# Performance work log

Hardware: AMD Instinct MI355X
Metric: run time of the kernel (lower is better)

The kernel has to match this reference:

```python
import jax, jax.numpy as jnp
import numpy as np

RADIUS = 0.2
MAX_SAMPLES = 9  # matches Conv2d kernel_size=[1, 9]


def ball_query(pcs, radius, nsample):
    """pcs: [B, 3, N] -> group_idx: [B, N, nsample] int32.
    First index of each group is the center point itself (distance 0)."""
    p = jnp.transpose(pcs, (0, 2, 1))  # [B, N, 3]
    sq = jnp.sum(p * p, axis=-1)  # [B, N]
    # pairwise squared distances [B, N, N]
    d2 = sq[:, :, None] + sq[:, None, :] - 2.0 * jnp.einsum('bnd,bmd->bnm', p, p)
    B, N, _ = d2.shape
    idx = jnp.broadcast_to(jnp.arange(N, dtype=jnp.int32), (B, N, N))
    idx = jnp.where(d2 > radius * radius, N, idx)  # out-of-ball -> sentinel N
    idx = jnp.sort(idx, axis=-1)[:, :, :nsample]  # in-ball indices first (ascending)
    first = idx[:, :, 0:1]  # center index (self, d2=0)
    idx = jnp.where(idx == N, first, idx)  # pad with center
    return idx


def setup_inputs() -> dict:
    key = jax.random.key(0)
    k1, k2, k3 = jax.random.split(key, 3)
    B, C_in, C_out, N = 4, 64, 128, 4096
    x = jax.random.normal(k1, (B, C_in, N), dtype=jnp.float32)
    pcs = jax.random.uniform(k2, (B, 3, N), dtype=jnp.float32)
    # Conv2d(in, out, [1, 9]) weight, xavier_uniform; bias zero-init
    fan_in = C_in * 1 * MAX_SAMPLES
    fan_out = C_out * 1 * MAX_SAMPLES
    limit = float(np.sqrt(6.0 / (fan_in + fan_out)))
    W = jax.random.uniform(k3, (C_out, C_in, MAX_SAMPLES), dtype=jnp.float32,
                           minval=-limit, maxval=limit)
    b = jnp.zeros((C_out,), dtype=jnp.float32)
    return {"x": x, "pcs": pcs, "W": W, "b": b}


def reference(x, pcs, W, b):
    """x: [B, C_in, N], pcs: [B, 3, N], W: [C_out, C_in, 9], b: [C_out].
    Returns y: [B, C_out, N]."""
    idx = ball_query(pcs, RADIUS, MAX_SAMPLES)  # [B, N, S]
    # gather grouped features: [B, C_in, N, S]
    x_grp = jnp.take_along_axis(x[:, :, None, :], idx[:, None, :, :], axis=3)
    # grouped, center-normalized coordinates (as in _group_points)
    pcs_grp = jnp.take_along_axis(pcs[:, :, None, :], idx[:, None, :, :], axis=3)
    pcs_grp = pcs_grp - pcs[:, :, :, None]  # [B, 3, N, S] (computed for fidelity)
    # Conv2d(in, out, [1, 9]) over [B, C_in, N, S] -> [B, C_out, N]
    y = jnp.einsum('bcns,ocs->bon', x_grp, W) + b[None, :, None]
    return y
```

## Files before the change

### kernel.cpp

```cpp
#include <hip/hip_runtime.h>

#define N_PTS 4096
#define B_SZ 4
#define C_IN 64
#define C_OUT 128
#define NS 9
#define KTOT (C_IN * NS)
#define RAD2 0.04f

typedef __attribute__((ext_vector_type(8))) short bf16x8;
typedef __attribute__((ext_vector_type(4))) float f32x4;

__device__ inline ushort f2bf(float f) {
    union { float f; unsigned u; } v; v.f = f;
    unsigned r = (v.u + 0x7FFF + ((v.u >> 16) & 1)) >> 16;
    return (ushort)r;
}

__device__ inline void gl_lds16(const void* g, void* l) {
    __builtin_amdgcn_global_load_lds(
        (const __attribute__((address_space(1))) unsigned int*)g,
        (__attribute__((address_space(3))) unsigned int*)l, 16, 0, 0);
}

#define LOADG(gi, qx, qy, qz) do {                                          \
    int mbase_ = (gi) * 256 + lane;                                         \
    _Pragma("unroll")                                                       \
    for (int j_ = 0; j_ < 4; ++j_) {                                        \
        int m_ = mbase_ + j_ * 64;                                          \
        qx[j_] = pb[m_]; qy[j_] = pb[N_PTS + m_]; qz[j_] = pb[2 * N_PTS + m_]; \
    }                                                                       \
} while (0)

#define PROCG(gi, qx, qy, qz) do {                                          \
    _Pragma("unroll")                                                       \
    for (int j_ = 0; j_ < 4; ++j_) {                                        \
        int m_ = (gi) * 256 + j_ * 64 + lane;                               \
        float sqm_ = __fadd_rn(__fadd_rn(__fmul_rn(qx[j_], qx[j_]),         \
                                         __fmul_rn(qy[j_], qy[j_])),        \
                               __fmul_rn(qz[j_], qz[j_]));                  \
        float dot_ = __fadd_rn(__fadd_rn(__fmul_rn(cx, qx[j_]),             \
                                         __fmul_rn(cy, qy[j_])),            \
                               __fmul_rn(cz, qz[j_]));                      \
        float d2_ = __fsub_rn(__fadd_rn(csq, sqm_), __fmul_rn(2.0f, dot_)); \
        bool hit_ = !(d2_ > RAD2);                                          \
        unsigned long long mask_ = __ballot(hit_);                          \
        if (mask_) {                                                        \
            if (first < 0) first = (gi) * 256 + j_ * 64 + __ffsll(mask_) - 1; \
            unsigned mlo_ = (unsigned)mask_, mhi_ = (unsigned)(mask_ >> 32); \
            int pre_ = __builtin_amdgcn_mbcnt_hi(mhi_,                      \
                           __builtin_amdgcn_mbcnt_lo(mlo_, 0));             \
            if (hit_) {                                                     \
                int slot_ = cnt + pre_;                                     \
                if (slot_ < NS) outb[(size_t)slot_ * N_PTS] = m_;           \
            }                                                               \
            cnt += __popcll(mask_);                                         \
        }                                                                   \
    }                                                                       \
} while (0)

__global__ void __launch_bounds__(256) prep_kernel(
    const float* __restrict__ W, const float* __restrict__ x,
    const float* __restrict__ pcs,
    ushort* __restrict__ Wt, ushort* __restrict__ xT, int* __restrict__ idxT)
{
    __shared__ ushort tile[64][66];
    const int t = threadIdx.x;
    const int blk = blockIdx.x;

    if (blk < 4096) {
        const int lane = t & 63;
        const int pt = t >> 6;
        const int widp = blk * 4 + pt;
        const int b = widp >> 12;
        const int n = widp & (N_PTS - 1);
        const float* pb = pcs + (size_t)b * 3 * N_PTS;
        float cx = pb[n], cy = pb[N_PTS + n], cz = pb[2 * N_PTS + n];
        float csq = __fadd_rn(__fadd_rn(__fmul_rn(cx, cx), __fmul_rn(cy, cy)),
                              __fmul_rn(cz, cz));
        int* outb = idxT + (size_t)b * NS * N_PTS + n;
        int cnt = 0, first = -1;
        float ax[4], ay[4], az[4], bx[4], by[4], bz[4];
        LOADG(0, ax, ay, az);
        #pragma unroll 1
        for (int g = 0; g < 16; g += 2) {
            if (g + 1 < 16) LOADG(g + 1, bx, by, bz);
            PROCG(g, ax, ay, az);
            if (cnt >= NS) break;
            if (g + 2 < 16) LOADG(g + 2, ax, ay, az);
            PROCG(g + 1, bx, by, bz);
            if (cnt >= NS) break;
        }
        if (lane >= cnt && lane < NS) outb[(size_t)lane * N_PTS] = first;
    } else if (blk < 4384) {
        int id = (blk - 4096) * 256 + t;
        int o = id / KTOT;
        int r = id - o * KTOT;
        int s = r >> 6, c = r & 63;
        int dst = o * KTOT + s * 64 + (((c >> 3) ^ (o & 7)) << 3) + (c & 7);
        Wt[dst] = f2bf(W[o * KTOT + c * NS + s]);
    } else {
        int r = blk - 4384;
        int b = r >> 6;
        int n0 = (r & 63) * 64;
        const float* xb = x + (size_t)b * C_IN * N_PTS;
        #pragma unroll
        for (int i = 0; i < 16; ++i) {
            int flat = i * 256 + t;
            int c = flat >> 6, n = flat & 63;
            tile[c][n] = f2bf(xb[(size_t)c * N_PTS + n0 + n]);
        }
        __syncthreads();
        ushort* xTb = xT + ((size_t)b * N_PTS + n0) * C_IN;
        #pragma unroll
        for (int i = 0; i < 16; ++i) {
            int flat = i * 256 + t;
            int n = flat >> 6, c = flat & 63;
            xTb[(size_t)n * C_IN + c] = tile[c][n];
        }
    }
}

__global__ void __launch_bounds__(512) conv_kernel(
    const ushort* __restrict__ xT, const ushort* __restrict__ Wt,
    const int* __restrict__ idxT, const float* __restrict__ bias,
    float* __restrict__ y)
{
    __shared__ __align__(16) ushort Wlds[64 * KTOT];
    __shared__ __align__(16) ushort Xlds[576 * 64];

    const int t = threadIdx.x;
    const int lane = t & 63;
    const int wid = t >> 6;
    const int ntile = blockIdx.x;
    const int b = blockIdx.y;
    const int n64 = ntile * 64;
    const int l15 = lane & 15;
    const int l4 = lane >> 4;

    const ushort* xTb = xT + (size_t)b * N_PTS * C_IN;
    const int* idxTb = idxT + (size_t)b * NS * N_PTS;

    const int rb = wid * 72;
    int g[9];
    #pragma unroll
    for (int j = 0; j < 9; ++j) {
        int r = rb + j * 8 + (lane >> 3);
        g[j] = idxTb[((r >> 6) << 12) + n64 + (r & 63)];
    }

    #pragma unroll
    for (int j = 0; j < 9; ++j) {
        int off = (wid * 9 + j) * 512 + lane * 8;
        gl_lds16(Wt + off, &Wlds[off]);
    }
    {
        const int sx = (((lane & 7) ^ (lane >> 3)) << 3);
        #pragma unroll
        for (int j = 0; j < 9; ++j)
            gl_lds16(xTb + ((size_t)g[j] << 6) + sx,
                     &Xlds[(rb + j * 8) * 64 + lane * 8]);
    }
    __syncthreads();

    const int m0 = (wid & 1) * 32;
    const int n0w = (wid >> 1) * 16;
    const int ra0 = m0 + l15;
    const int rb0 = n0w + l15;
    const int swA = ra0 & 7;
    const int swB = rb0 & 7;
    float* yb = y + (size_t)b * C_OUT * N_PTS + n64;

    #pragma unroll
    for (int half = 0; half < 2; ++half) {
        f32x4 acc[2];
        acc[0] = (f32x4){0.f, 0.f, 0.f, 0.f};
        acc[1] = (f32x4){0.f, 0.f, 0.f, 0.f};

        #pragma unroll
        for (int s = 0; s < NS; ++s) {
            #pragma unroll
            for (int hh = 0; hh < 2; ++hh) {
                int d = hh * 4 + l4;
                bf16x8 a0 = *(const bf16x8*)&Wlds[ra0 * KTOT + s * 64 + ((d ^ swA) << 3)];
                bf16x8 a1 = *(const bf16x8*)&Wlds[(ra0 + 16) * KTOT + s * 64 + ((d ^ swA) << 3)];
                bf16x8 b0 = *(const bf16x8*)&Xlds[(s * 64 + rb0) * 64 + ((d ^ swB) << 3)];
                acc[0] = __builtin_amdgcn_mfma_f32_16x16x32_bf16(a0, b0, acc[0], 0, 0, 0);
                acc[1] = __builtin_amdgcn_mfma_f32_16x16x32_bf16(a1, b0, acc[1], 0, 0, 0);
            }
        }

        #pragma unroll
        for (int fm = 0; fm < 2; ++fm) {
            #pragma unroll
            for (int j = 0; j < 4; ++j) {
                int o = half * 64 + m0 + fm * 16 + l4 * 4 + j;
                yb[(size_t)o * N_PTS + n0w + l15] = acc[fm][j] + bias[o];
            }
        }

        if (half == 0) {
            __syncthreads();
            #pragma unroll
            for (int j = 0; j < 9; ++j) {
                int off = (wid * 9 + j) * 512 + lane * 8;
                gl_lds16(Wt + 36864 + off, &Wlds[off]);
            }
            __syncthreads();
        }
    }
}

extern "C" void kernel_launch(void* const* d_in, const int* in_sizes, int n_in,
                              void* d_out, int out_size, void* d_ws, size_t ws_size,
                              hipStream_t stream) {
    const float* x    = (const float*)d_in[0];
    const float* pcs  = (const float*)d_in[1];
    const float* W    = (const float*)d_in[2];
    const float* bias = (const float*)d_in[3];
    float* y = (float*)d_out;

    int*    idxT = (int*)d_ws;
    ushort* xT   = (ushort*)((char*)d_ws + 851968);
    ushort* Wt   = (ushort*)((char*)d_ws + 2949120);

    prep_kernel<<<4640, 256, 0, stream>>>(W, x, pcs, Wt, xT, idxT);
    conv_kernel<<<dim3(64, B_SZ), 512, 0, stream>>>(xT, Wt, idxT, bias, y);
}
```

Measured before the change: 20.58 us.

## Precompute packed float4 points with squared norms in a separate ball-query kernel

The prep kernel now packs each point as a float4 (x, y, z, |p|^2) into workspace. Ball query moves into its own kernel that reads these packed points with one vector load and no per-candidate norm computation. This cuts scattered scalar loads and per-candidate arithmetic, at the cost of an extra kernel launch and a dependency between the two kernels. The x transpose and W conversion no longer share a launch with the ball query.

```diff
diff --git a/kernel.cpp b/kernel.cpp
--- a/kernel.cpp
+++ b/kernel.cpp
@@ -23,26 +23,65 @@
         (__attribute__((address_space(3))) unsigned int*)l, 16, 0, 0);
 }
 
-#define LOADG(gi, qx, qy, qz) do {                                          \
+__global__ void __launch_bounds__(256) prep_kernel(
+    const float* __restrict__ W, const float* __restrict__ x,
+    const float* __restrict__ pcs,
+    ushort* __restrict__ Wt, ushort* __restrict__ xT, float4* __restrict__ pp)
+{
+    __shared__ ushort tile[64][66];
+    const int t = threadIdx.x;
+    const int blk = blockIdx.x;
+    if (blk < 288) {
+        int id = blk * 256 + t;
+        int o = id / KTOT;
+        int r = id - o * KTOT;
+        int s = r >> 6, c = r & 63;
+        int dst = o * KTOT + s * 64 + (((c >> 3) ^ (o & 7)) << 3) + (c & 7);
+        Wt[dst] = f2bf(W[o * KTOT + c * NS + s]);
+    } else if (blk < 544) {
+        int r = blk - 288;
+        int b = r >> 6;
+        int n0 = (r & 63) * 64;
+        const float* xb = x + (size_t)b * C_IN * N_PTS;
+        #pragma unroll
+        for (int i = 0; i < 16; ++i) {
+            int flat = i * 256 + t;
+            int c = flat >> 6, n = flat & 63;
+            tile[c][n] = f2bf(xb[(size_t)c * N_PTS + n0 + n]);
+        }
+        __syncthreads();
+        ushort* xTb = xT + ((size_t)b * N_PTS + n0) * C_IN;
+        #pragma unroll
+        for (int i = 0; i < 16; ++i) {
+            int flat = i * 256 + t;
+            int n = flat >> 6, c = flat & 63;
+            xTb[(size_t)n * C_IN + c] = tile[c][n];
+        }
+    } else {
+        int id = (blk - 544) * 256 + t;
+        int b = id >> 12, n = id & (N_PTS - 1);
+        const float* pb = pcs + (size_t)b * 3 * N_PTS;
+        float px = pb[n], py = pb[N_PTS + n], pz = pb[2 * N_PTS + n];
+        float sq = __fadd_rn(__fadd_rn(__fmul_rn(px, px), __fmul_rn(py, py)),
+                             __fmul_rn(pz, pz));
+        pp[id] = make_float4(px, py, pz, sq);
+    }
+}
+
+#define LOADG(gi, q) do {                                                   \
     int mbase_ = (gi) * 256 + lane;                                         \
     _Pragma("unroll")                                                       \
-    for (int j_ = 0; j_ < 4; ++j_) {                                        \
-        int m_ = mbase_ + j_ * 64;                                          \
-        qx[j_] = pb[m_]; qy[j_] = pb[N_PTS + m_]; qz[j_] = pb[2 * N_PTS + m_]; \
-    }                                                                       \
+    for (int j_ = 0; j_ < 4; ++j_) q[j_] = pb4[mbase_ + j_ * 64];           \
 } while (0)
 
-#define PROCG(gi, qx, qy, qz) do {                                          \
+#define PROCG(gi, q) do {                                                   \
     _Pragma("unroll")                                                       \
     for (int j_ = 0; j_ < 4; ++j_) {                                        \
         int m_ = (gi) * 256 + j_ * 64 + lane;                               \
-        float sqm_ = __fadd_rn(__fadd_rn(__fmul_rn(qx[j_], qx[j_]),         \
-                                         __fmul_rn(qy[j_], qy[j_])),        \
-                               __fmul_rn(qz[j_], qz[j_]));                  \
-        float dot_ = __fadd_rn(__fadd_rn(__fmul_rn(cx, qx[j_]),             \
-                                         __fmul_rn(cy, qy[j_])),            \
-                               __fmul_rn(cz, qz[j_]));                      \
-        float d2_ = __fsub_rn(__fadd_rn(csq, sqm_), __fmul_rn(2.0f, dot_)); \
+        float dot_ = __fadd_rn(__fadd_rn(__fmul_rn(cx, q[j_].x),            \
+                                         __fmul_rn(cy, q[j_].y)),           \
+                               __fmul_rn(cz, q[j_].z));                     \
+        float d2_ = __fsub_rn(__fadd_rn(csq, q[j_].w), __fmul_rn(2.0f, dot_)); \
         bool hit_ = !(d2_ > RAD2);                                          \
         unsigned long long mask_ = __ballot(hit_);                          \
         if (mask_) {                                                        \
@@ -59,66 +98,29 @@
     }                                                                       \
 } while (0)
 
-__global__ void __launch_bounds__(256) prep_kernel(
-    const float* __restrict__ W, const float* __restrict__ x,
-    const float* __restrict__ pcs,
-    ushort* __restrict__ Wt, ushort* __restrict__ xT, int* __restrict__ idxT)
-{
-    __shared__ ushort tile[64][66];
-    const int t = threadIdx.x;
-    const int blk = blockIdx.x;
-
-    if (blk < 4096) {
-        const int lane = t & 63;
-        const int pt = t >> 6;
-        const int widp = blk * 4 + pt;
-        const int b = widp >> 12;
-        const int n = widp & (N_PTS - 1);
-        const float* pb = pcs + (size_t)b * 3 * N_PTS;
-        float cx = pb[n], cy = pb[N_PTS + n], cz = pb[2 * N_PTS + n];
-        float csq = __fadd_rn(__fadd_rn(__fmul_rn(cx, cx), __fmul_rn(cy, cy)),
-                              __fmul_rn(cz, cz));
-        int* outb = idxT + (size_t)b * NS * N_PTS + n;
-        int cnt = 0, first = -1;
-        float ax[4], ay[4], az[4], bx[4], by[4], bz[4];
-        LOADG(0, ax, ay, az);
-        #pragma unroll 1
-        for (int g = 0; g < 16; g += 2) {
-            if (g + 1 < 16) LOADG(g + 1, bx, by, bz);
-            PROCG(g, ax, ay, az);
-            if (cnt >= NS) break;
-            if (g + 2 < 16) LOADG(g + 2, ax, ay, az);
-            PROCG(g + 1, bx, by, bz);
-            if (cnt >= NS) break;
-        }
-        if (lane >= cnt && lane < NS) outb[(size_t)lane * N_PTS] = first;
-    } else if (blk < 4384) {
-        int id = (blk - 4096) * 256 + t;
-        int o = id / KTOT;
-        int r = id - o * KTOT;
-        int s = r >> 6, c = r & 63;
-        int dst = o * KTOT + s * 64 + (((c >> 3) ^ (o & 7)) << 3) + (c & 7);
-        Wt[dst] = f2bf(W[o * KTOT + c * NS + s]);
-    } else {
-        int r = blk - 4384;
-        int b = r >> 6;
-        int n0 = (r & 63) * 64;
-        const float* xb = x + (size_t)b * C_IN * N_PTS;
-        #pragma unroll
-        for (int i = 0; i < 16; ++i) {
-            int flat = i * 256 + t;
-            int c = flat >> 6, n = flat & 63;
-            tile[c][n] = f2bf(xb[(size_t)c * N_PTS + n0 + n]);
-        }
-        __syncthreads();
-        ushort* xTb = xT + ((size_t)b * N_PTS + n0) * C_IN;
-        #pragma unroll
-        for (int i = 0; i < 16; ++i) {
-            int flat = i * 256 + t;
-            int n = flat >> 6, c = flat & 63;
-            xTb[(size_t)n * C_IN + c] = tile[c][n];
-        }
-    }
+__global__ void __launch_bounds__(256) ballq_kernel(const float4* __restrict__ pp,
+                                                    int* __restrict__ idxT) {
+    const int lane = threadIdx.x & 63;
+    const int widp = blockIdx.x * 4 + (threadIdx.x >> 6);
+    const int b = widp >> 12;
+    const int n = widp & (N_PTS - 1);
+    const float4* pb4 = pp + (size_t)b * N_PTS;
+    float4 c = pb4[n];
+    const float cx = c.x, cy = c.y, cz = c.z, csq = c.w;
+    int* outb = idxT + (size_t)b * NS * N_PTS + n;
+    int cnt = 0, first = -1;
+    float4 qa[4], qb[4];
+    LOADG(0, qa);
+    #pragma unroll 1
+    for (int g = 0; g < 16; g += 2) {
+        if (g + 1 < 16) LOADG(g + 1, qb);
+        PROCG(g, qa);
+        if (cnt >= NS) break;
+        if (g + 2 < 16) LOADG(g + 2, qa);
+        PROCG(g + 1, qb);
+        if (cnt >= NS) break;
+    }
+    if (lane >= cnt && lane < NS) outb[(size_t)lane * N_PTS] = first;
 }
 
 __global__ void __launch_bounds__(512) conv_kernel(
@@ -221,9 +223,11 @@
     float* y = (float*)d_out;
 
     int*    idxT = (int*)d_ws;
+    float4* pp   = (float4*)((char*)d_ws + 589824);
     ushort* xT   = (ushort*)((char*)d_ws + 851968);
     ushort* Wt   = (ushort*)((char*)d_ws + 2949120);
 
-    prep_kernel<<<4640, 256, 0, stream>>>(W, x, pcs, Wt, xT, idxT);
+    prep_kernel<<<608, 256, 0, stream>>>(W, x, pcs, Wt, xT, pp);
+    ballq_kernel<<<4096, 256, 0, stream>>>(pp, idxT);
     conv_kernel<<<dim3(64, B_SZ), 512, 0, stream>>>(xT, Wt, idxT, bias, y);
 }
```

Result: slower. 26.74 us (+29.9%).
